# Kernel tuning notes

Measured on AMD Instinct MI355X. Metric: run time of the kernel, lower is better.

Reference implementation:

```python
import jax, jax.numpy as jnp
import numpy as np

# DeepSeek-V2-Lite MoE dims
E = 64      # n_routed_experts
H = 2048    # hidden_size
I = 1408    # moe_intermediate_size
K = 6       # num_experts_per_tok (top-k)
T = 1024    # tokens
C = 256     # per-expert capacity (expected load T*K/E = 96; 256 is ample, no drops with seed 0)


def setup_inputs() -> dict:
    key = jax.random.key(0)
    k1, k2, k3, k4 = jax.random.split(key, 4)
    return {
        "hidden_states": jax.random.normal(k1, (T, H), jnp.float32),
        "gate_w": jax.random.normal(k2, (H, E), jnp.float32) * 0.02,   # LiteLinear(H->E), no bias
        "w1": jax.random.normal(k3, (E, H, I), jnp.float32) * 0.02,    # experts_w1
        "w2": jax.random.normal(k4, (E, I, H), jnp.float32) * 0.02,    # experts_w2
    }


def _moe(x, gate_w, w1, w2):
    # Router: softmax gate + top-k + renormalize (vLLM fused_moe renormalize=True)
    logits = x @ gate_w                                    # [T, E]
    probs = jax.nn.softmax(logits, axis=-1)
    topk_w, topk_idx = jax.lax.top_k(probs, K)             # [T, K]
    topk_w = topk_w / jnp.sum(topk_w, axis=-1, keepdims=True)

    # Dispatch: flatten (token, k) pairs, compute slot position within each expert
    P = T * K
    e_p = topk_idx.reshape(P)                              # expert id per pair
    onehot = (e_p[:, None] == jnp.arange(E)[None, :]).astype(jnp.int32)  # [P, E]
    pos = jnp.cumsum(onehot, axis=0) - 1                   # running count per expert
    pos = jnp.take_along_axis(pos, e_p[:, None], axis=1)[:, 0]           # [P]
    valid = pos < C
    pos_c = jnp.where(valid, pos, 0)
    fvalid = valid[:, None].astype(x.dtype)

    x_pair = jnp.repeat(x, K, axis=0)                      # [P, H]
    xe = jnp.zeros((E, C, H), x.dtype).at[e_p, pos_c].add(x_pair * fvalid)  # [E, C, H]

    # Grouped expert GEMMs: silu(x @ w1) @ w2
    h = jax.nn.silu(jnp.einsum('ech,ehi->eci', xe, w1))    # [E, C, I]
    ye = jnp.einsum('eci,eih->ech', h, w2)                 # [E, C, H]

    # Combine: gather back per pair, weight by routing prob, sum over k
    y_pair = ye[e_p, pos_c] * fvalid                       # [P, H]
    out = (y_pair.reshape(T, K, H) * topk_w[..., None]).sum(axis=1)
    return out


def reference(hidden_states, gate_w, w1, w2):
    return _moe(hidden_states, gate_w, w1, w2)
```

## Files before the change

kernel.cpp:

```cpp
#include <hip/hip_runtime.h>

#define T_TOK 1024
#define H_DIM 2048
#define I_DIM 1408
#define E_NUM 64
#define K_TOP 6
#define CAP   256
#define P_NUM (T_TOK * K_TOP)
#define ROWS_MAX 7168

typedef __bf16 bf16x8 __attribute__((ext_vector_type(8)));
typedef float  f32x4  __attribute__((ext_vector_type(4)));

__global__ void zero_out_kernel(float* __restrict__ out) {
    int i = blockIdx.x * 256 + threadIdx.x;
    ((f32x4*)out)[i] = (f32x4){0.f, 0.f, 0.f, 0.f};
}

__global__ void zerocnt_kernel(int* __restrict__ cnt) {
    if (threadIdx.x < E_NUM) cnt[threadIdx.x] = 0;
}

__global__ __launch_bounds__(256) void router_kernel(
        const float* __restrict__ x, const float* __restrict__ gw,
        float* __restrict__ tw, int* __restrict__ ti, __bf16* __restrict__ xb)
{
    const int t0  = blockIdx.x * 4;
    const int tid = threadIdx.x;
    __shared__ float xs[4][H_DIM];
    __shared__ float part[4][4][E_NUM];

    #pragma unroll
    for (int tt = 0; tt < 4; ++tt) {
        #pragma unroll
        for (int i = 0; i < 8; ++i) {
            float v = x[(size_t)(t0 + tt) * H_DIM + i * 256 + tid];
            xs[tt][i * 256 + tid] = v;
            xb[(size_t)(t0 + tt) * H_DIM + i * 256 + tid] = (__bf16)v;
        }
    }
    __syncthreads();

    const int e = tid & 63, q = tid >> 6;
    float a0 = 0.f, a1 = 0.f, a2 = 0.f, a3 = 0.f;
    for (int hh = q * 512; hh < q * 512 + 512; ++hh) {
        float g = gw[hh * E_NUM + e];
        a0 += xs[0][hh] * g; a1 += xs[1][hh] * g;
        a2 += xs[2][hh] * g; a3 += xs[3][hh] * g;
    }
    part[q][0][e] = a0; part[q][1][e] = a1; part[q][2][e] = a2; part[q][3][e] = a3;
    __syncthreads();

    const int tt = q;
    float l = part[0][tt][e] + part[1][tt][e] + part[2][tt][e] + part[3][tt][e];
    float m = l;
    #pragma unroll
    for (int s = 32; s; s >>= 1) m = fmaxf(m, __shfl_xor(m, s));
    float p = __expf(l - m);
    float sum = p;
    #pragma unroll
    for (int s = 32; s; s >>= 1) sum += __shfl_xor(sum, s);
    float prob = p / sum;

    float v = prob, wsum = 0.f;
    float tv[K_TOP]; int tix[K_TOP];
    #pragma unroll
    for (int k = 0; k < K_TOP; ++k) {
        float bv = v; int bi = e;
        #pragma unroll
        for (int s = 32; s; s >>= 1) {
            float ov = __shfl_xor(bv, s); int oi = __shfl_xor(bi, s);
            if (ov > bv || (ov == bv && oi < bi)) { bv = ov; bi = oi; }
        }
        tv[k] = bv; tix[k] = bi; wsum += bv;
        if (e == bi) v = -1.0f;
    }
    if (e == 0) {
        #pragma unroll
        for (int k = 0; k < K_TOP; ++k) {
            tw[(t0 + tt) * K_TOP + k] = tv[k] / wsum;
            ti[(t0 + tt) * K_TOP + k] = tix[k];
        }
    }
}

__global__ void dispatch_kernel(const int* __restrict__ ti, int* __restrict__ cnt,
                                int* __restrict__ list) {
    int p = blockIdx.x * 256 + threadIdx.x;
    if (p < P_NUM) {
        int e = ti[p];
        int slot = atomicAdd(&cnt[e], 1);
        if (slot < CAP) list[e * CAP + slot] = p;
    }
}

__global__ void scan_kernel(const int* __restrict__ cnt, int* __restrict__ base) {
    if (threadIdx.x == 0) {
        int acc = 0;
        for (int e = 0; e < E_NUM; ++e) {
            base[e] = acc;
            int c = cnt[e]; if (c > CAP) c = CAP;
            acc += (c + 15) & ~15;
        }
    }
}

__global__ __launch_bounds__(256, 2) void gemm1_kernel(
        const float* __restrict__ w1, const __bf16* __restrict__ xb,
        const int* __restrict__ cnt, const int* __restrict__ base,
        const int* __restrict__ list, __bf16* __restrict__ hbuf)
{
    const int e  = blockIdx.z;
    const int m0 = blockIdx.y * 128;
    const int nb = blockIdx.x * 128;

    int rows = cnt[e]; if (rows > CAP) rows = CAP;
    const int rows_pad = (rows + 15) & ~15;
    if (m0 >= rows_pad) return;
    int mcount = rows_pad - m0; if (mcount > 128) mcount = 128;
    const int nmf = mcount >> 4;
    const int hb = base[e];

    __shared__ __attribute__((aligned(16))) __bf16 As[128][72];
    __shared__ int ts[128];

    const int tid = threadIdx.x;
    if (tid < 128) {
        int slot = m0 + tid;
        ts[tid] = (slot < rows) ? (list[e * CAP + slot] / K_TOP) : 0;
    }
    __syncthreads();

    const int lane = tid & 63;
    const int wv   = tid >> 6;
    const int l15  = lane & 15;
    const int lg   = lane >> 4;
    const int nw   = nb + wv * 32;

    const int sm = tid >> 3;
    const int sk = (tid & 7) << 3;

    const __bf16* ap[4];
    #pragma unroll
    for (int it = 0; it < 4; ++it)
        ap[it] = xb + (size_t)ts[it * 32 + sm] * H_DIM + sk;

    const float* wbase = w1 + (size_t)e * H_DIM * I_DIM
                            + (size_t)(lg * 8) * I_DIM + (nw + l15);

    f32x4 acc[8][2];
    #pragma unroll
    for (int m = 0; m < 8; ++m) {
        acc[m][0] = (f32x4){0.f, 0.f, 0.f, 0.f};
        acc[m][1] = (f32x4){0.f, 0.f, 0.f, 0.f};
    }

    for (int k0 = 0; k0 < H_DIM; k0 += 64) {
        bf16x8 bfr[2][2];
        #pragma unroll
        for (int ks = 0; ks < 2; ++ks) {
            const float* bp = wbase + (size_t)(k0 + ks * 32) * I_DIM;
            #pragma unroll
            for (int nf = 0; nf < 2; ++nf) {
                #pragma unroll
                for (int j = 0; j < 8; ++j)
                    bfr[ks][nf][j] = (__bf16)bp[(size_t)j * I_DIM + nf * 16];
            }
        }
        __syncthreads();
        #pragma unroll
        for (int it = 0; it < 4; ++it) {
            bf16x8 v = *(const bf16x8*)(ap[it] + k0);
            *(bf16x8*)(&As[it * 32 + sm][sk]) = v;
        }
        __syncthreads();
        #pragma unroll
        for (int ks = 0; ks < 2; ++ks) {
            #pragma unroll
            for (int m = 0; m < 8; ++m) {
                if (m < nmf) {
                    bf16x8 a = *(const bf16x8*)(&As[m * 16 + l15][ks * 32 + lg * 8]);
                    acc[m][0] = __builtin_amdgcn_mfma_f32_16x16x32_bf16(a, bfr[ks][0], acc[m][0], 0, 0, 0);
                    acc[m][1] = __builtin_amdgcn_mfma_f32_16x16x32_bf16(a, bfr[ks][1], acc[m][1], 0, 0, 0);
                }
            }
        }
    }

    #pragma unroll
    for (int m = 0; m < 8; ++m) {
        if (m < nmf) {
            #pragma unroll
            for (int nf = 0; nf < 2; ++nf) {
                #pragma unroll
                for (int j = 0; j < 4; ++j) {
                    int row = m * 16 + lg * 4 + j;
                    int col = nw + nf * 16 + l15;
                    float v = acc[m][nf][j];
                    float s = v / (1.0f + __expf(-v));
                    hbuf[(size_t)(hb + m0 + row) * I_DIM + col] = (__bf16)s;
                }
            }
        }
    }
}

__global__ __launch_bounds__(256, 2) void gemm2_kernel(
        const float* __restrict__ w2, const __bf16* __restrict__ hbuf,
        const int* __restrict__ cnt, const int* __restrict__ base,
        const int* __restrict__ list, const float* __restrict__ tw,
        float* __restrict__ out)
{
    const int e  = blockIdx.z;
    const int m0 = blockIdx.y * 128;
    const int nb = blockIdx.x * 128;

    int rows = cnt[e]; if (rows > CAP) rows = CAP;
    const int rows_pad = (rows + 15) & ~15;
    if (m0 >= rows_pad) return;
    int mcount = rows_pad - m0; if (mcount > 128) mcount = 128;
    const int nmf = mcount >> 4;
    const int hb = base[e];

    __shared__ __attribute__((aligned(16))) __bf16 As[128][72];
    __shared__ int ps[128];
    __shared__ float tws[128];

    const int tid = threadIdx.x;
    if (tid < 128) {
        int slot = m0 + tid;
        int p = (slot < rows) ? list[e * CAP + slot] : -1;
        ps[tid] = p;
        tws[tid] = (p >= 0) ? tw[p] : 0.f;
    }

    const int lane = tid & 63;
    const int wv   = tid >> 6;
    const int l15  = lane & 15;
    const int lg   = lane >> 4;
    const int nw   = nb + wv * 32;

    const int sm = tid >> 3;
    const int sk = (tid & 7) << 3;

    const __bf16* abase = hbuf + (size_t)(hb + m0 + sm) * I_DIM + sk;
    const float*  wbase = w2 + (size_t)e * I_DIM * H_DIM
                             + (size_t)(lg * 8) * H_DIM + (nw + l15);

    f32x4 acc[8][2];
    #pragma unroll
    for (int m = 0; m < 8; ++m) {
        acc[m][0] = (f32x4){0.f, 0.f, 0.f, 0.f};
        acc[m][1] = (f32x4){0.f, 0.f, 0.f, 0.f};
    }

    for (int k0 = 0; k0 < I_DIM; k0 += 64) {
        bf16x8 bfr[2][2];
        #pragma unroll
        for (int ks = 0; ks < 2; ++ks) {
            const float* bp = wbase + (size_t)(k0 + ks * 32) * H_DIM;
            #pragma unroll
            for (int nf = 0; nf < 2; ++nf) {
                #pragma unroll
                for (int j = 0; j < 8; ++j)
                    bfr[ks][nf][j] = (__bf16)bp[(size_t)j * H_DIM + nf * 16];
            }
        }
        __syncthreads();
        #pragma unroll
        for (int it = 0; it < 4; ++it) {
            bf16x8 v = *(const bf16x8*)(abase + (size_t)(it * 32) * I_DIM + k0);
            *(bf16x8*)(&As[it * 32 + sm][sk]) = v;
        }
        __syncthreads();
        #pragma unroll
        for (int ks = 0; ks < 2; ++ks) {
            #pragma unroll
            for (int m = 0; m < 8; ++m) {
                if (m < nmf) {
                    bf16x8 a = *(const bf16x8*)(&As[m * 16 + l15][ks * 32 + lg * 8]);
                    acc[m][0] = __builtin_amdgcn_mfma_f32_16x16x32_bf16(a, bfr[ks][0], acc[m][0], 0, 0, 0);
                    acc[m][1] = __builtin_amdgcn_mfma_f32_16x16x32_bf16(a, bfr[ks][1], acc[m][1], 0, 0, 0);
                }
            }
        }
    }

    #pragma unroll
    for (int m = 0; m < 8; ++m) {
        if (m < nmf) {
            #pragma unroll
            for (int nf = 0; nf < 2; ++nf) {
                #pragma unroll
                for (int j = 0; j < 4; ++j) {
                    int row = m * 16 + lg * 4 + j;
                    int p = ps[row];
                    if (p >= 0) {
                        int t = p / K_TOP;
                        float v = acc[m][nf][j] * tws[row];
                        atomicAdd(&out[(size_t)t * H_DIM + (nw + nf * 16 + l15)], v);
                    }
                }
            }
        }
    }
}

extern "C" void kernel_launch(void* const* d_in, const int* in_sizes, int n_in,
                              void* d_out, int out_size, void* d_ws, size_t ws_size,
                              hipStream_t stream) {
    const float* x  = (const float*)d_in[0];
    const float* gw = (const float*)d_in[1];
    const float* w1 = (const float*)d_in[2];
    const float* w2 = (const float*)d_in[3];
    float* out = (float*)d_out;

    char* ws = (char*)d_ws;
    int*    cnt  = (int*)ws;
    int*    base = (int*)(ws + 256);
    int*    list = (int*)(ws + 512);
    float*  tw   = (float*)(ws + 66048);
    int*    ti   = (int*)(ws + 90624);
    __bf16* xb   = (__bf16*)(ws + 131072);
    __bf16* hbuf = (__bf16*)(ws + 4325376);

    hipLaunchKernelGGL(zero_out_kernel, dim3(T_TOK * H_DIM / 4 / 256), dim3(256), 0, stream, out);
    hipLaunchKernelGGL(zerocnt_kernel, dim3(1), dim3(64), 0, stream, cnt);
    hipLaunchKernelGGL(router_kernel, dim3(T_TOK / 4), dim3(256), 0, stream,
                       x, gw, tw, ti, xb);
    hipLaunchKernelGGL(dispatch_kernel, dim3((P_NUM + 255) / 256), dim3(256), 0, stream,
                       ti, cnt, list);
    hipLaunchKernelGGL(scan_kernel, dim3(1), dim3(64), 0, stream, cnt, base);
    hipLaunchKernelGGL(gemm1_kernel, dim3(I_DIM / 128, 2, E_NUM), dim3(256), 0, stream,
                       w1, xb, cnt, base, list, hbuf);
    hipLaunchKernelGGL(gemm2_kernel, dim3(H_DIM / 128, 2, E_NUM), dim3(256), 0, stream,
                       w2, hbuf, cnt, base, list, tw, out);
}
```

Measured before the change: 509.4 us.

## Stage fp32 weights via vectorized loads into swizzled LDS with double-buffered prefetch

The expert GEMMs now load fp32 weight tiles with 16-byte vector loads, convert them to bf16 and store them in a swizzled shared-memory B tile, instead of doing strided scalar loads per lane. Activation and weight loads for the next k-step are prefetched in registers while the current step runs its MFMAs. N tiles shrink to 64 columns with a 2x2 wave layout, and occupancy is raised to 4 blocks per CU. Dispatch and scan are fused into one single-block kernel using shared-memory atomics, which removes the counter-zeroing and scan launches. The cost is extra barriers per step, higher register pressure, and serial dispatch work in one block.

After: 532.6 us. +4.6%, slower.

```diff
diff --git a/kernel.cpp b/kernel.cpp
--- a/kernel.cpp
+++ b/kernel.cpp
@@ -7,18 +7,20 @@
 #define K_TOP 6
 #define CAP   256
 #define P_NUM (T_TOK * K_TOP)
-#define ROWS_MAX 7168
 
 typedef __bf16 bf16x8 __attribute__((ext_vector_type(8)));
 typedef float  f32x4  __attribute__((ext_vector_type(4)));
+typedef unsigned int uint32x2 __attribute__((ext_vector_type(2)));
+
+__device__ inline unsigned pack2bf16(float a, float b) {
+    unsigned short au = __builtin_bit_cast(unsigned short, (__bf16)a);
+    unsigned short bu = __builtin_bit_cast(unsigned short, (__bf16)b);
+    return (unsigned)au | ((unsigned)bu << 16);
+}
 
 __global__ void zero_out_kernel(float* __restrict__ out) {
     int i = blockIdx.x * 256 + threadIdx.x;
     ((f32x4*)out)[i] = (f32x4){0.f, 0.f, 0.f, 0.f};
-}
-
-__global__ void zerocnt_kernel(int* __restrict__ cnt) {
-    if (threadIdx.x < E_NUM) cnt[threadIdx.x] = 0;
 }
 
 __global__ __launch_bounds__(256) void router_kernel(
@@ -84,35 +86,125 @@
     }
 }
 
-__global__ void dispatch_kernel(const int* __restrict__ ti, int* __restrict__ cnt,
-                                int* __restrict__ list) {
-    int p = blockIdx.x * 256 + threadIdx.x;
-    if (p < P_NUM) {
+__global__ __launch_bounds__(1024) void dispatch_scan_kernel(
+        const int* __restrict__ ti, int* __restrict__ cnt,
+        int* __restrict__ base, int* __restrict__ list)
+{
+    __shared__ int lcnt[E_NUM];
+    const int tid = threadIdx.x;
+    if (tid < E_NUM) lcnt[tid] = 0;
+    __syncthreads();
+    #pragma unroll
+    for (int i = 0; i < P_NUM / 1024; ++i) {
+        int p = i * 1024 + tid;
         int e = ti[p];
-        int slot = atomicAdd(&cnt[e], 1);
+        int slot = atomicAdd(&lcnt[e], 1);
         if (slot < CAP) list[e * CAP + slot] = p;
     }
-}
-
-__global__ void scan_kernel(const int* __restrict__ cnt, int* __restrict__ base) {
-    if (threadIdx.x == 0) {
+    __syncthreads();
+    if (tid == 0) {
         int acc = 0;
         for (int e = 0; e < E_NUM; ++e) {
             base[e] = acc;
-            int c = cnt[e]; if (c > CAP) c = CAP;
+            int c = lcnt[e];
+            cnt[e] = c;
+            if (c > CAP) c = CAP;
             acc += (c + 15) & ~15;
         }
     }
 }
 
-__global__ __launch_bounds__(256, 2) void gemm1_kernel(
+#define B_LDB 36
+
+
+#define GEMM_BODY(LD, NSTEP_, APTR_EXPR)                                        \
+    f32x4 f0[4], f1[4]; bf16x8 av0[4], av1[4];                                  \
+                                        \
+    {                                                                           \
+        const float* bp = bload;                                                \
+        _Pragma("unroll")                                                       \
+        for (int r = 0; r < 4; ++r) f0[r] = *(const f32x4*)(bp + (size_t)r * LD);\
+        _Pragma("unroll")                                                       \
+        for (int it = 0; it < 4; ++it) av0[it] = *(const bf16x8*)(ap[it]);      \
+        bp = bload + (size_t)64 * LD;                                           \
+        _Pragma("unroll")                                                       \
+        for (int r = 0; r < 4; ++r) f1[r] = *(const f32x4*)(bp + (size_t)r * LD);\
+        _Pragma("unroll")                                                       \
+        for (int it = 0; it < 4; ++it) av1[it] = *(const bf16x8*)(ap[it] + 64); \
+    }                                                                           \
+    for (int t = 0; t < NSTEP_; t += 2) {                                       \
+                 \
+        __syncthreads();                                                        \
+        _Pragma("unroll")                                                       \
+        for (int it = 0; it < 4; ++it)                                          \
+            *(bf16x8*)(&As[it * 32 + sm][sk]) = av0[it];                        \
+        _Pragma("unroll")                                                       \
+        for (int i = 0; i < 4; ++i) {                                           \
+            unsigned lo = pack2bf16(f0[0][i], f0[1][i]);                        \
+            unsigned hi = pack2bf16(f0[2][i], f0[3][i]);                        \
+            *(uint32x2*)(&Bs[(4 * c4 + i) * B_LDB + ((2 * kq) ^ Xw)]) =         \
+                (uint32x2){lo, hi};                                             \
+        }                                                                       \
+        if (t + 2 < NSTEP_) {                                                   \
+            int kn = (t + 2) * 64;                                              \
+            const float* bp = bload + (size_t)kn * LD;                          \
+            _Pragma("unroll")                                                   \
+            for (int r = 0; r < 4; ++r) f0[r] = *(const f32x4*)(bp + (size_t)r * LD);\
+            _Pragma("unroll")                                                   \
+            for (int it = 0; it < 4; ++it) av0[it] = *(const bf16x8*)(ap[it] + kn);\
+        }                                                                       \
+        __syncthreads();                                                        \
+        MFMA_PHASE();                                                           \
+               \
+        __syncthreads();                                                        \
+        _Pragma("unroll")                                                       \
+        for (int it = 0; it < 4; ++it)                                          \
+            *(bf16x8*)(&As[it * 32 + sm][sk]) = av1[it];                        \
+        _Pragma("unroll")                                                       \
+        for (int i = 0; i < 4; ++i) {                                           \
+            unsigned lo = pack2bf16(f1[0][i], f1[1][i]);                        \
+            unsigned hi = pack2bf16(f1[2][i], f1[3][i]);                        \
+            *(uint32x2*)(&Bs[(4 * c4 + i) * B_LDB + ((2 * kq) ^ Xw)]) =         \
+                (uint32x2){lo, hi};                                             \
+        }                                                                       \
+        if (t + 3 < NSTEP_) {                                                   \
+            int kn = (t + 3) * 64;                                              \
+            const float* bp = bload + (size_t)kn * LD;                          \
+            _Pragma("unroll")                                                   \
+            for (int r = 0; r < 4; ++r) f1[r] = *(const f32x4*)(bp + (size_t)r * LD);\
+            _Pragma("unroll")                                                   \
+            for (int it = 0; it < 4; ++it) av1[it] = *(const bf16x8*)(ap[it] + kn);\
+        }                                                                       \
+        __syncthreads();                                                        \
+        MFMA_PHASE();                                                           \
+    }
+
+#define MFMA_PHASE()                                                            \
+    {                                                                           \
+        _Pragma("unroll")                                                       \
+        for (int ks = 0; ks < 2; ++ks) {                                        \
+            int pbase = ks * 16 + lg * 4;                                       \
+            bf16x8 b0 = *(const bf16x8*)(&Bs[cB0 * B_LDB + (pbase ^ Xr0)]);     \
+            bf16x8 b1 = *(const bf16x8*)(&Bs[cB1 * B_LDB + (pbase ^ Xr1)]);     \
+            _Pragma("unroll")                                                   \
+            for (int m = 0; m < 4; ++m) {                                       \
+                if (wm * 4 + m < nmf) {                                         \
+                    bf16x8 a = *(const bf16x8*)(&As[wm * 64 + m * 16 + l15][ks * 32 + lg * 8]);\
+                    acc[m][0] = __builtin_amdgcn_mfma_f32_16x16x32_bf16(a, b0, acc[m][0], 0, 0, 0);\
+                    acc[m][1] = __builtin_amdgcn_mfma_f32_16x16x32_bf16(a, b1, acc[m][1], 0, 0, 0);\
+                }                                                               \
+            }                                                                   \
+        }                                                                       \
+    }
+
+__global__ __launch_bounds__(256, 4) void gemm1_kernel(
         const float* __restrict__ w1, const __bf16* __restrict__ xb,
         const int* __restrict__ cnt, const int* __restrict__ base,
         const int* __restrict__ list, __bf16* __restrict__ hbuf)
 {
     const int e  = blockIdx.z;
     const int m0 = blockIdx.y * 128;
-    const int nb = blockIdx.x * 128;
+    const int nb = blockIdx.x * 64;
 
     int rows = cnt[e]; if (rows > CAP) rows = CAP;
     const int rows_pad = (rows + 15) & ~15;
@@ -122,6 +214,7 @@
     const int hb = base[e];
 
     __shared__ __attribute__((aligned(16))) __bf16 As[128][72];
+    __shared__ __attribute__((aligned(16))) unsigned Bs[64 * B_LDB];
     __shared__ int ts[128];
 
     const int tid = threadIdx.x;
@@ -135,66 +228,46 @@
     const int wv   = tid >> 6;
     const int l15  = lane & 15;
     const int lg   = lane >> 4;
-    const int nw   = nb + wv * 32;
+    const int wm   = wv >> 1;
+    const int wn   = wv & 1;
 
     const int sm = tid >> 3;
     const int sk = (tid & 7) << 3;
-
     const __bf16* ap[4];
     #pragma unroll
     for (int it = 0; it < 4; ++it)
         ap[it] = xb + (size_t)ts[it * 32 + sm] * H_DIM + sk;
 
-    const float* wbase = w1 + (size_t)e * H_DIM * I_DIM
-                            + (size_t)(lg * 8) * I_DIM + (nw + l15);
-
-    f32x4 acc[8][2];
-    #pragma unroll
-    for (int m = 0; m < 8; ++m) {
+    const int c4 = tid & 15;
+    const int kq = tid >> 4;
+    const int Xw = 4 * ((c4 ^ (c4 >> 3)) & 7);
+    const float* bload = w1 + (size_t)e * H_DIM * I_DIM
+                            + (size_t)(4 * kq) * I_DIM + (nb + 4 * c4);
+
+    const int cB0 = wn * 32 + l15;
+    const int cB1 = cB0 + 16;
+    const int c4r0 = cB0 >> 2, c4r1 = cB1 >> 2;
+    const int Xr0 = 4 * ((c4r0 ^ (c4r0 >> 3)) & 7);
+    const int Xr1 = 4 * ((c4r1 ^ (c4r1 >> 3)) & 7);
+
+    f32x4 acc[4][2];
+    #pragma unroll
+    for (int m = 0; m < 4; ++m) {
         acc[m][0] = (f32x4){0.f, 0.f, 0.f, 0.f};
         acc[m][1] = (f32x4){0.f, 0.f, 0.f, 0.f};
     }
 
-    for (int k0 = 0; k0 < H_DIM; k0 += 64) {
-        bf16x8 bfr[2][2];
-        #pragma unroll
-        for (int ks = 0; ks < 2; ++ks) {
-            const float* bp = wbase + (size_t)(k0 + ks * 32) * I_DIM;
-            #pragma unroll
-            for (int nf = 0; nf < 2; ++nf) {
-                #pragma unroll
-                for (int j = 0; j < 8; ++j)
-                    bfr[ks][nf][j] = (__bf16)bp[(size_t)j * I_DIM + nf * 16];
-            }
-        }
-        __syncthreads();
-        #pragma unroll
-        for (int it = 0; it < 4; ++it) {
-            bf16x8 v = *(const bf16x8*)(ap[it] + k0);
-            *(bf16x8*)(&As[it * 32 + sm][sk]) = v;
-        }
-        __syncthreads();
-        #pragma unroll
-        for (int ks = 0; ks < 2; ++ks) {
-            #pragma unroll
-            for (int m = 0; m < 8; ++m) {
-                if (m < nmf) {
-                    bf16x8 a = *(const bf16x8*)(&As[m * 16 + l15][ks * 32 + lg * 8]);
-                    acc[m][0] = __builtin_amdgcn_mfma_f32_16x16x32_bf16(a, bfr[ks][0], acc[m][0], 0, 0, 0);
-                    acc[m][1] = __builtin_amdgcn_mfma_f32_16x16x32_bf16(a, bfr[ks][1], acc[m][1], 0, 0, 0);
-                }
-            }
-        }
-    }
-
-    #pragma unroll
-    for (int m = 0; m < 8; ++m) {
-        if (m < nmf) {
+    GEMM_BODY(I_DIM, (H_DIM / 64), )
+
+    const int nw = nb + wn * 32;
+    #pragma unroll
+    for (int m = 0; m < 4; ++m) {
+        if (wm * 4 + m < nmf) {
             #pragma unroll
             for (int nf = 0; nf < 2; ++nf) {
                 #pragma unroll
                 for (int j = 0; j < 4; ++j) {
-                    int row = m * 16 + lg * 4 + j;
+                    int row = wm * 64 + m * 16 + lg * 4 + j;
                     int col = nw + nf * 16 + l15;
                     float v = acc[m][nf][j];
                     float s = v / (1.0f + __expf(-v));
@@ -205,7 +278,7 @@
     }
 }
 
-__global__ __launch_bounds__(256, 2) void gemm2_kernel(
+__global__ __launch_bounds__(256, 4) void gemm2_kernel(
         const float* __restrict__ w2, const __bf16* __restrict__ hbuf,
         const int* __restrict__ cnt, const int* __restrict__ base,
         const int* __restrict__ list, const float* __restrict__ tw,
@@ -213,7 +286,7 @@
 {
     const int e  = blockIdx.z;
     const int m0 = blockIdx.y * 128;
-    const int nb = blockIdx.x * 128;
+    const int nb = blockIdx.x * 64;
 
     int rows = cnt[e]; if (rows > CAP) rows = CAP;
     const int rows_pad = (rows + 15) & ~15;
@@ -223,6 +296,7 @@
     const int hb = base[e];
 
     __shared__ __attribute__((aligned(16))) __bf16 As[128][72];
+    __shared__ __attribute__((aligned(16))) unsigned Bs[64 * B_LDB];
     __shared__ int ps[128];
     __shared__ float tws[128];
 
@@ -238,62 +312,46 @@
     const int wv   = tid >> 6;
     const int l15  = lane & 15;
     const int lg   = lane >> 4;
-    const int nw   = nb + wv * 32;
+    const int wm   = wv >> 1;
+    const int wn   = wv & 1;
 
     const int sm = tid >> 3;
     const int sk = (tid & 7) << 3;
-
-    const __bf16* abase = hbuf + (size_t)(hb + m0 + sm) * I_DIM + sk;
-    const float*  wbase = w2 + (size_t)e * I_DIM * H_DIM
-                             + (size_t)(lg * 8) * H_DIM + (nw + l15);
-
-    f32x4 acc[8][2];
-    #pragma unroll
-    for (int m = 0; m < 8; ++m) {
+    const __bf16* ap[4];
+    #pragma unroll
+    for (int it = 0; it < 4; ++it)
+        ap[it] = hbuf + (size_t)(hb + m0 + it * 32 + sm) * I_DIM + sk;
+
+    const int c4 = tid & 15;
+    const int kq = tid >> 4;
+    const int Xw = 4 * ((c4 ^ (c4 >> 3)) & 7);
+    const float* bload = w2 + (size_t)e * I_DIM * H_DIM
+                            + (size_t)(4 * kq) * H_DIM + (nb + 4 * c4);
+
+    const int cB0 = wn * 32 + l15;
+    const int cB1 = cB0 + 16;
+    const int c4r0 = cB0 >> 2, c4r1 = cB1 >> 2;
+    const int Xr0 = 4 * ((c4r0 ^ (c4r0 >> 3)) & 7);
+    const int Xr1 = 4 * ((c4r1 ^ (c4r1 >> 3)) & 7);
+
+    f32x4 acc[4][2];
+    #pragma unroll
+    for (int m = 0; m < 4; ++m) {
         acc[m][0] = (f32x4){0.f, 0.f, 0.f, 0.f};
         acc[m][1] = (f32x4){0.f, 0.f, 0.f, 0.f};
     }
 
-    for (int k0 = 0; k0 < I_DIM; k0 += 64) {
-        bf16x8 bfr[2][2];
-        #pragma unroll
-        for (int ks = 0; ks < 2; ++ks) {
-            const float* bp = wbase + (size_t)(k0 + ks * 32) * H_DIM;
-            #pragma unroll
-            for (int nf = 0; nf < 2; ++nf) {
-                #pragma unroll
-                for (int j = 0; j < 8; ++j)
-                    bfr[ks][nf][j] = (__bf16)bp[(size_t)j * H_DIM + nf * 16];
-            }
-        }
-        __syncthreads();
-        #pragma unroll
-        for (int it = 0; it < 4; ++it) {
-            bf16x8 v = *(const bf16x8*)(abase + (size_t)(it * 32) * I_DIM + k0);
-            *(bf16x8*)(&As[it * 32 + sm][sk]) = v;
-        }
-        __syncthreads();
-        #pragma unroll
-        for (int ks = 0; ks < 2; ++ks) {
-            #pragma unroll
-            for (int m = 0; m < 8; ++m) {
-                if (m < nmf) {
-                    bf16x8 a = *(const bf16x8*)(&As[m * 16 + l15][ks * 32 + lg * 8]);
-                    acc[m][0] = __builtin_amdgcn_mfma_f32_16x16x32_bf16(a, bfr[ks][0], acc[m][0], 0, 0, 0);
-                    acc[m][1] = __builtin_amdgcn_mfma_f32_16x16x32_bf16(a, bfr[ks][1], acc[m][1], 0, 0, 0);
-                }
-            }
-        }
-    }
-
-    #pragma unroll
-    for (int m = 0; m < 8; ++m) {
-        if (m < nmf) {
+    GEMM_BODY(H_DIM, (I_DIM / 64), )
+
+    const int nw = nb + wn * 32;
+    #pragma unroll
+    for (int m = 0; m < 4; ++m) {
+        if (wm * 4 + m < nmf) {
             #pragma unroll
             for (int nf = 0; nf < 2; ++nf) {
                 #pragma unroll
                 for (int j = 0; j < 4; ++j) {
-                    int row = m * 16 + lg * 4 + j;
+                    int row = wm * 64 + m * 16 + lg * 4 + j;
                     int p = ps[row];
                     if (p >= 0) {
                         int t = p / K_TOP;
@@ -325,14 +383,12 @@
     __bf16* hbuf = (__bf16*)(ws + 4325376);
 
     hipLaunchKernelGGL(zero_out_kernel, dim3(T_TOK * H_DIM / 4 / 256), dim3(256), 0, stream, out);
-    hipLaunchKernelGGL(zerocnt_kernel, dim3(1), dim3(64), 0, stream, cnt);
     hipLaunchKernelGGL(router_kernel, dim3(T_TOK / 4), dim3(256), 0, stream,
                        x, gw, tw, ti, xb);
-    hipLaunchKernelGGL(dispatch_kernel, dim3((P_NUM + 255) / 256), dim3(256), 0, stream,
-                       ti, cnt, list);
-    hipLaunchKernelGGL(scan_kernel, dim3(1), dim3(64), 0, stream, cnt, base);
-    hipLaunchKernelGGL(gemm1_kernel, dim3(I_DIM / 128, 2, E_NUM), dim3(256), 0, stream,
+    hipLaunchKernelGGL(dispatch_scan_kernel, dim3(1), dim3(1024), 0, stream,
+                       ti, cnt, base, list);
+    hipLaunchKernelGGL(gemm1_kernel, dim3(I_DIM / 64, 2, E_NUM), dim3(256), 0, stream,
                        w1, xb, cnt, base, list, hbuf);
-    hipLaunchKernelGGL(gemm2_kernel, dim3(H_DIM / 128, 2, E_NUM), dim3(256), 0, stream,
+    hipLaunchKernelGGL(gemm2_kernel, dim3(H_DIM / 64, 2, E_NUM), dim3(256), 0, stream,
                        w2, hbuf, cnt, base, list, tw, out);
 }
```
